# Optimization experiments

Measured on AMD Instinct MI355X. Metric: run time of the kernel, lower is better.

## Reference

```python
import jax, jax.numpy as jnp
import numpy as np

N_LEVELS = 16
N_FEATURES = 2
MIN_RES = 16
MAX_RES = 512
HASH_SIZE = 19
TABLE_SIZE = 2 ** HASH_SIZE
# per-level grid resolutions (geometric progression, matches torch buffer)
RESOLUTIONS = [int(MIN_RES * (MAX_RES / MIN_RES) ** (i / (N_LEVELS - 1))) for i in range(N_LEVELS)]
# 8 cube-corner offsets, [8, 3] (same ordering as torch.meshgrid indexing='ij')
OFFSETS = np.stack(np.meshgrid(np.array([0, 1]), np.array([0, 1]), np.array([0, 1]), indexing='ij')).reshape(3, -1).T.astype(np.int64)
PRIMES = np.array([1, 2654435761, 805459861], dtype=np.int64)


def setup_inputs() -> dict:
    key = jax.random.key(0)
    k1, k2 = jax.random.split(key)
    N = 1 << 20  # ~1M sample points (e.g., 4096 rays x 256 samples)
    x = jax.random.uniform(k1, (N, 3), dtype=jnp.float32, minval=-1.0, maxval=1.0)
    tables = jax.random.uniform(k2, (N_LEVELS, TABLE_SIZE, N_FEATURES), dtype=jnp.float32, minval=-1e-4, maxval=1e-4)
    return {"x": x, "tables": tables}


def reference(x, tables):
    x = jnp.clip(x.astype(jnp.float32), -1.0, 1.0)  # [N, 3]
    offsets = jnp.asarray(OFFSETS)                  # [8, 3] int64
    primes = jnp.asarray(PRIMES)                    # [3] int64
    outs = []
    for i, res in enumerate(RESOLUTIONS):
        coords = x * res                            # [N, 3]
        cf = jnp.floor(coords)
        lc = coords - cf                            # fractional part, [N, 3]
        # 8 corner integer coords, wrapped into [0, res): [N, 8, 3]
        corners = (cf.astype(jnp.int64)[:, None, :] + offsets[None]) % res
        corners_f = corners.astype(jnp.float32) / res
        # spatial hash: quantize to [0, 2^18) grid then prime-multiply hash
        q = ((corners_f + 1.0) * 0.5 * (2.0 ** 18)).astype(jnp.int64)
        hashed = (q * primes).sum(-1) % TABLE_SIZE  # [N, 8]
        feats = tables[i][hashed]                   # gather, [N, 8, F]
        # trilinear weights: prod over dims of (1-lc) if offset==0 else lc
        w = jnp.where(offsets[None] == 0, 1.0 - lc[:, None, :], lc[:, None, :]).prod(-1)  # [N, 8]
        outs.append((w[..., None] * feats).sum(1))  # [N, F]
    return jnp.concatenate(outs, axis=-1)           # [N, L*F]
```

## Files before the change

kernel.cpp:

```cpp
#include <hip/hip_runtime.h>


static constexpr int      kNLevels   = 16;
static constexpr unsigned kTableSize = 1u << 19;
static constexpr unsigned kMask      = kTableSize - 1u;
static constexpr unsigned kP1        = 2654435761u;
static constexpr unsigned kP2        = 805459861u;

static constexpr int kNBins = 32768;

typedef float v4f __attribute__((ext_vector_type(4)));
typedef float v2f __attribute__((ext_vector_type(2)));

constexpr int RES_[kNLevels]  = {16, 20, 25, 32, 40, 50, 64, 80,
                                 101, 127, 161, 203, 256, 322, 406, 512};
constexpr int QOFF_[kNLevels] = {0, 16, 36, 61, 93, 133, 183, 247,
                                 327, 428, 555, 716, 919, 1175, 1497, 1903};
static constexpr int kQTot = 2415;

constexpr unsigned qval_rcp(int c, int res) {
    const float r = 1.0f / (float)res;
    const float v = (float)c * r;
    const float s = ((v + 1.0f) * 0.5f) * 262144.0f;
    return (unsigned)s;
}

struct QTab {
    unsigned v[kQTot];
    constexpr QTab() : v{} {
        int o = 0;
        for (int i = 0; i < kNLevels; ++i) {
            for (int c = 0; c < RES_[i]; ++c) v[o + c] = qval_rcp(c, RES_[i]);
            o += RES_[i];
        }
    }
};
__constant__ QTab QT = QTab();

__device__ __forceinline__ void level_idx_w_rt(
    const int res, const unsigned* __restrict__ qt,
    const float px, const float py, const float pz,
    unsigned* __restrict__ idx, float* __restrict__ w)
{
    const float resf = (float)res;

    const float cxf = px * resf, cyf = py * resf, czf = pz * resf;
    const float fx = floorf(cxf), fy = floorf(cyf), fz = floorf(czf);
    const float lx = cxf - fx, ly = cyf - fy, lz = czf - fz;

    const int ix = (int)fx, iy = (int)fy, iz = (int)fz;
    const int cx0 = ix < 0 ? ix + res : (ix >= res ? ix - res : ix);
    const int cy0 = iy < 0 ? iy + res : (iy >= res ? iy - res : iy);
    const int cz0 = iz < 0 ? iz + res : (iz >= res ? iz - res : iz);
    const int cx1 = (cx0 + 1 == res) ? 0 : cx0 + 1;
    const int cy1 = (cy0 + 1 == res) ? 0 : cy0 + 1;
    const int cz1 = (cz0 + 1 == res) ? 0 : cz0 + 1;

    const unsigned qx0 = qt[cx0], qx1 = qt[cx1];
    const unsigned qy0 = qt[cy0], qy1 = qt[cy1];
    const unsigned qz0 = qt[cz0], qz1 = qt[cz1];

    const unsigned hy0 = qy0 * kP1, hy1 = qy1 * kP1;
    const unsigned hz0 = qz0 * kP2, hz1 = qz1 * kP2;

    const float wx0 = 1.0f - lx, wx1 = lx;
    const float wy0 = 1.0f - ly, wy1 = ly;
    const float wz0 = 1.0f - lz, wz1 = lz;

#pragma unroll
    for (int m = 0; m < 8; ++m) {
        const unsigned h = ((m & 4) ? qx1 : qx0) +
                           ((m & 2) ? hy1 : hy0) +
                           ((m & 1) ? hz1 : hz0);
        idx[m] = h & kMask;
        w[m] = (((m & 4) ? wx1 : wx0) * ((m & 2) ? wy1 : wy0)) *
               ((m & 1) ? wz1 : wz0);
    }
}

__device__ __forceinline__ unsigned spread5(unsigned x) {
    x &= 0x3ffu;
    x = (x | (x << 16)) & 0x30000FFu;
    x = (x | (x << 8))  & 0x300F00Fu;
    x = (x | (x << 4))  & 0x30C30C3u;
    x = (x | (x << 2))  & 0x9249249u;
    return x;
}

__device__ __forceinline__ unsigned point_bin(const float* __restrict__ x, int n) {
    float px = fminf(fmaxf(x[3 * n + 0], -1.0f), 1.0f);
    float py = fminf(fmaxf(x[3 * n + 1], -1.0f), 1.0f);
    float pz = fminf(fmaxf(x[3 * n + 2], -1.0f), 1.0f);
    int cx = (int)((px + 1.0f) * 16.0f); cx = cx > 31 ? 31 : cx;
    int cy = (int)((py + 1.0f) * 16.0f); cy = cy > 31 ? 31 : cy;
    int cz = (int)((pz + 1.0f) * 16.0f); cz = cz > 31 ? 31 : cz;
    return spread5((unsigned)cx) | (spread5((unsigned)cy) << 1) |
           (spread5((unsigned)cz) << 2);
}

__global__ void zero_kernel(unsigned* __restrict__ p, int n) {
    int i = blockIdx.x * 256 + threadIdx.x;
    if (i < n) p[i] = 0u;
}

__global__ void hist_kernel(const float* __restrict__ x,
                            unsigned* __restrict__ counts, int N) {
    int n = blockIdx.x * 256 + threadIdx.x;
    if (n >= N) return;
    atomicAdd(&counts[point_bin(x, n)], 1u);
}

__global__ __launch_bounds__(1024) void scan_kernel(
    const unsigned* __restrict__ counts, unsigned* __restrict__ cursor) {
    __shared__ unsigned sh[1024];
    const int t = threadIdx.x;
    unsigned loc[32];
    unsigned s = 0;
#pragma unroll
    for (int j = 0; j < 32; ++j) { loc[j] = s; s += counts[t * 32 + j]; }
    sh[t] = s;
    __syncthreads();
    for (int off = 1; off < 1024; off <<= 1) {
        unsigned v = (t >= off) ? sh[t - off] : 0u;
        __syncthreads();
        sh[t] += v;
        __syncthreads();
    }
    const unsigned base = sh[t] - s;
#pragma unroll
    for (int j = 0; j < 32; ++j) cursor[t * 32 + j] = base + loc[j];
}

__global__ void scatter_kernel(const float* __restrict__ x,
                               unsigned* __restrict__ cursor,
                               v4f* __restrict__ xs, int N) {
    int n = blockIdx.x * 256 + threadIdx.x;
    if (n >= N) return;
    unsigned pos = atomicAdd(&cursor[point_bin(x, n)], 1u);
    v4f v = {x[3 * n + 0], x[3 * n + 1], x[3 * n + 2], __int_as_float(n)};
    xs[pos] = v;
}

__global__ __launch_bounds__(256, 5) void hashenc_sorted_kernel(
    const v4f* __restrict__ xs,
    const float* __restrict__ tables,
    float* __restrict__ out,
    int N)
{
    __shared__ unsigned sq[kQTot];
    for (int t = threadIdx.x; t < kQTot; t += 256) sq[t] = QT.v[t];
    __syncthreads();

    int bid = blockIdx.x;
    const int nblk = gridDim.x;
    if ((nblk & 7) == 0) bid = (bid & 7) * (nblk >> 3) + (bid >> 3);

    const int g = bid * 256 + threadIdx.x;
    if (g >= N) return;

    const v4f p = xs[g];
    const int n = __float_as_int(p.w);

    float px = fminf(fmaxf(p.x, -1.0f), 1.0f);
    float py = fminf(fmaxf(p.y, -1.0f), 1.0f);
    float pz = fminf(fmaxf(p.z, -1.0f), 1.0f);

    v4f* op = (v4f*)(out + (size_t)n * (2 * kNLevels));

#pragma unroll
    for (int q = 0; q < 8; ++q) {
        const int iA = 2 * q, iB = 2 * q + 1;

        unsigned ia[8], ib[8];
        float    wa[8], wb[8];
        level_idx_w_rt(RES_[iA], sq + QOFF_[iA], px, py, pz, ia, wa);
        level_idx_w_rt(RES_[iB], sq + QOFF_[iB], px, py, pz, ib, wb);

        const v2f* tA = (const v2f*)tables + (size_t)iA * kTableSize;
        const v2f* tB = (const v2f*)tables + (size_t)iB * kTableSize;

        v2f fa[8], fb[8];
#pragma unroll
        for (int m = 0; m < 8; ++m) {
            const v2f* a = tA + ia[m];
            asm volatile("global_load_dwordx2 %0, %1, off"
                         : "=v"(fa[m]) : "v"(a));
        }
#pragma unroll
        for (int m = 0; m < 8; ++m) {
            const v2f* a = tB + ib[m];
            asm volatile("global_load_dwordx2 %0, %1, off"
                         : "=v"(fb[m]) : "v"(a));
        }
        asm volatile("s_waitcnt vmcnt(0)" ::: "memory");
        __builtin_amdgcn_sched_barrier(0);

        float a0 = 0.0f, a1 = 0.0f, b0 = 0.0f, b1 = 0.0f;
#pragma unroll
        for (int m = 0; m < 8; ++m) {
            a0 += wa[m] * fa[m].x;
            a1 += wa[m] * fa[m].y;
        }
#pragma unroll
        for (int m = 0; m < 8; ++m) {
            b0 += wb[m] * fb[m].x;
            b1 += wb[m] * fb[m].y;
        }

        v4f v = {a0, a1, b0, b1};
        op[q] = v;
    }
}

__global__ __launch_bounds__(256, 6) void hashenc_full_kernel(
    const float* __restrict__ x,
    const float* __restrict__ tables,
    float* __restrict__ out,
    int N)
{
    __shared__ unsigned sq[kQTot];
    for (int t = threadIdx.x; t < kQTot; t += 256) sq[t] = QT.v[t];
    __syncthreads();

    const int n = blockIdx.x * 256 + threadIdx.x;
    if (n >= N) return;

    float px = x[3 * n + 0];
    float py = x[3 * n + 1];
    float pz = x[3 * n + 2];
    px = fminf(fmaxf(px, -1.0f), 1.0f);
    py = fminf(fmaxf(py, -1.0f), 1.0f);
    pz = fminf(fmaxf(pz, -1.0f), 1.0f);

    v4f* op = (v4f*)(out + (size_t)n * (2 * kNLevels));

#pragma unroll
    for (int ip = 0; ip < kNLevels / 2; ++ip) {
        const int iA = 2 * ip, iB = 2 * ip + 1;

        unsigned ia[8], ib[8];
        float    wa[8], wb[8];
        level_idx_w_rt(RES_[iA], sq + QOFF_[iA], px, py, pz, ia, wa);
        level_idx_w_rt(RES_[iB], sq + QOFF_[iB], px, py, pz, ib, wb);

        const v2f* tA = (const v2f*)tables + (size_t)iA * kTableSize;
        const v2f* tB = (const v2f*)tables + (size_t)iB * kTableSize;

        v2f fa[8], fb[8];
#pragma unroll
        for (int m = 0; m < 8; ++m) fa[m] = tA[ia[m]];
#pragma unroll
        for (int m = 0; m < 8; ++m) fb[m] = tB[ib[m]];

        float a0 = 0.0f, a1 = 0.0f, b0 = 0.0f, b1 = 0.0f;
#pragma unroll
        for (int m = 0; m < 8; ++m) {
            a0 += wa[m] * fa[m].x;
            a1 += wa[m] * fa[m].y;
        }
#pragma unroll
        for (int m = 0; m < 8; ++m) {
            b0 += wb[m] * fb[m].x;
            b1 += wb[m] * fb[m].y;
        }

        v4f v = {a0, a1, b0, b1};
        op[ip] = v;
    }
}

extern "C" void kernel_launch(void* const* d_in, const int* in_sizes, int n_in,
                              void* d_out, int out_size, void* d_ws, size_t ws_size,
                              hipStream_t stream) {
    const float* x      = (const float*)d_in[0];
    const float* tables = (const float*)d_in[1];
    float*       out    = (float*)d_out;
    const int N = in_sizes[0] / 3;
    const int pb = (N + 255) / 256;

    const size_t need = (size_t)2 * kNBins * sizeof(unsigned)
                      + (size_t)N * sizeof(v4f);
    if (d_ws != nullptr && ws_size >= need) {
        unsigned* counts = (unsigned*)d_ws;
        unsigned* cursor = counts + kNBins;
        v4f*      xs     = (v4f*)(cursor + kNBins);

        hipLaunchKernelGGL(zero_kernel, dim3((kNBins + 255) / 256), dim3(256),
                           0, stream, counts, kNBins);
        hipLaunchKernelGGL(hist_kernel, dim3(pb), dim3(256), 0, stream,
                           x, counts, N);
        hipLaunchKernelGGL(scan_kernel, dim3(1), dim3(1024), 0, stream,
                           counts, cursor);
        hipLaunchKernelGGL(scatter_kernel, dim3(pb), dim3(256), 0, stream,
                           x, cursor, xs, N);
        hipLaunchKernelGGL(hashenc_sorted_kernel, dim3(pb), dim3(256),
                           0, stream, xs, tables, out, N);
    } else {
        hipLaunchKernelGGL(hashenc_full_kernel, dim3(pb), dim3(256),
                           0, stream, x, tables, out, N);
    }
}
```

Measured before the change: 993.3 us.

## Software-pipeline hash gathers across levels with a three-stage register ring

Restructures the sorted hash-encoding kernel to process one level at a time. Table gathers for the next two levels are issued while the current level's weights are applied, with partial vmcnt waits instead of a full drain after every pair of levels. The goal is to keep more gather latency hidden within each wave. Because a ring of three levels' features and weights must stay in registers, the launch-bounds occupancy target drops from 5 to 4 blocks, which costs some latency hiding from wave switching.

Measured after the change: 975.9 us. No clear change (-1.8%).

```diff
diff --git a/kernel.cpp b/kernel.cpp
--- a/kernel.cpp
+++ b/kernel.cpp
@@ -75,6 +75,23 @@
         idx[m] = h & kMask;
         w[m] = (((m & 4) ? wx1 : wx0) * ((m & 2) ? wy1 : wy0)) *
                ((m & 1) ? wz1 : wz0);
+    }
+}
+
+__device__ __forceinline__ void prep_issue(
+    const int lv, const unsigned* __restrict__ sq,
+    const float* __restrict__ tables,
+    const float px, const float py, const float pz,
+    v2f* __restrict__ fdst, float* __restrict__ wdst)
+{
+    unsigned idx[8];
+    level_idx_w_rt(RES_[lv], sq + QOFF_[lv], px, py, pz, idx, wdst);
+    const v2f* tb = (const v2f*)tables + (size_t)lv * kTableSize;
+#pragma unroll
+    for (int m = 0; m < 8; ++m) {
+        const v2f* a = tb + idx[m];
+        asm volatile("global_load_dwordx2 %0, %1, off"
+                     : "=v"(fdst[m]) : "v"(a));
     }
 }
 
@@ -141,7 +158,7 @@
     xs[pos] = v;
 }
 
-__global__ __launch_bounds__(256, 5) void hashenc_sorted_kernel(
+__global__ __launch_bounds__(256, 4) void hashenc_sorted_kernel(
     const v4f* __restrict__ xs,
     const float* __restrict__ tables,
     float* __restrict__ out,
@@ -167,48 +184,40 @@
 
     v4f* op = (v4f*)(out + (size_t)n * (2 * kNLevels));
 
-#pragma unroll
-    for (int q = 0; q < 8; ++q) {
-        const int iA = 2 * q, iB = 2 * q + 1;
-
-        unsigned ia[8], ib[8];
-        float    wa[8], wb[8];
-        level_idx_w_rt(RES_[iA], sq + QOFF_[iA], px, py, pz, ia, wa);
-        level_idx_w_rt(RES_[iB], sq + QOFF_[iB], px, py, pz, ib, wb);
-
-        const v2f* tA = (const v2f*)tables + (size_t)iA * kTableSize;
-        const v2f* tB = (const v2f*)tables + (size_t)iB * kTableSize;
-
-        v2f fa[8], fb[8];
+    v2f   f[3][8];
+    float w[3][8];
+
+    prep_issue(0, sq, tables, px, py, pz, f[0], w[0]);
+    prep_issue(1, sq, tables, px, py, pz, f[1], w[1]);
+
+    float pa0 = 0.0f, pa1 = 0.0f;
+#pragma unroll
+    for (int i = 0; i < kNLevels; ++i) {
+        if (i + 2 < kNLevels)
+            prep_issue(i + 2, sq, tables, px, py, pz,
+                       f[(i + 2) % 3], w[(i + 2) % 3]);
+
+        if (i + 2 < kNLevels)
+            asm volatile("s_waitcnt vmcnt(16)" ::: "memory");
+        else if (i + 1 < kNLevels)
+            asm volatile("s_waitcnt vmcnt(8)" ::: "memory");
+        else
+            asm volatile("s_waitcnt vmcnt(0)" ::: "memory");
+        __builtin_amdgcn_sched_barrier(0);
+
+        const int s = i % 3;
+        float a0 = 0.0f, a1 = 0.0f;
 #pragma unroll
         for (int m = 0; m < 8; ++m) {
-            const v2f* a = tA + ia[m];
-            asm volatile("global_load_dwordx2 %0, %1, off"
-                         : "=v"(fa[m]) : "v"(a));
-        }
-#pragma unroll
-        for (int m = 0; m < 8; ++m) {
-            const v2f* a = tB + ib[m];
-            asm volatile("global_load_dwordx2 %0, %1, off"
-                         : "=v"(fb[m]) : "v"(a));
-        }
-        asm volatile("s_waitcnt vmcnt(0)" ::: "memory");
-        __builtin_amdgcn_sched_barrier(0);
-
-        float a0 = 0.0f, a1 = 0.0f, b0 = 0.0f, b1 = 0.0f;
-#pragma unroll
-        for (int m = 0; m < 8; ++m) {
-            a0 += wa[m] * fa[m].x;
-            a1 += wa[m] * fa[m].y;
-        }
-#pragma unroll
-        for (int m = 0; m < 8; ++m) {
-            b0 += wb[m] * fb[m].x;
-            b1 += wb[m] * fb[m].y;
-        }
-
-        v4f v = {a0, a1, b0, b1};
-        op[q] = v;
+            a0 += w[s][m] * f[s][m].x;
+            a1 += w[s][m] * f[s][m].y;
+        }
+        if (i & 1) {
+            v4f v = {pa0, pa1, a0, a1};
+            op[i >> 1] = v;
+        } else {
+            pa0 = a0; pa1 = a1;
+        }
     }
 }
 
```
